# Kernel tuning notes

Hardware: AMD Instinct MI355X
Metric: run time of the kernel (lower is better)

## Reference

```python
import jax, jax.numpy as jnp
import numpy as np

NUM_HEAD_CHANNELS = 64
GROUPS = 32
EPS = 1e-5


def setup_inputs() -> dict:
    key = jax.random.key(0)
    ks = jax.random.split(key, 3)
    B, C, H, W = 16, 512, 64, 64
    x = jax.random.normal(ks[0], (B, C, H, W), jnp.float32)
    gn_gamma = jnp.ones((C,), jnp.float32)
    gn_beta = jnp.zeros((C,), jnp.float32)
    # 1x1 conv weights (out_ch, in_ch); fan-in scaling keeps softmax logits sane
    w_qkv = jax.random.normal(ks[1], (3 * C, C), jnp.float32) / np.float32(np.sqrt(C))
    b_qkv = jnp.zeros((3 * C,), jnp.float32)
    w_proj = jax.random.normal(ks[2], (C, C), jnp.float32) / np.float32(np.sqrt(C))
    b_proj = jnp.zeros((C,), jnp.float32)
    return dict(x=x, gn_gamma=gn_gamma, gn_beta=gn_beta, w_qkv=w_qkv,
                b_qkv=b_qkv, w_proj=w_proj, b_proj=b_proj)


def _group_norm(x, gamma, beta):
    B, C, H, W = x.shape
    xg = x.reshape(B, GROUPS, C // GROUPS, H, W)
    mu = xg.mean(axis=(2, 3, 4), keepdims=True)
    var = xg.var(axis=(2, 3, 4), keepdims=True)
    xn = ((xg - mu) * jax.lax.rsqrt(var + EPS)).reshape(B, C, H, W)
    return xn * gamma[None, :, None, None] + beta[None, :, None, None]


def reference(x, gn_gamma, gn_beta, w_qkv, b_qkv, w_proj, b_proj):
    B, C, H, W = x.shape
    L = H * W
    heads = C // NUM_HEAD_CHANNELS
    Lh = L // heads  # module splits spatial length across heads

    xn = _group_norm(x, gn_gamma, gn_beta).reshape(B, C, L)
    # 1x1 conv QKV: (3C, C) x (B, C, L) -> (B, 3C, L)
    qkv = jnp.einsum('oc,bcl->bol', w_qkv, xn) + b_qkv[None, :, None]
    qkv = qkv.reshape(B, 3 * C, heads, Lh)
    q, k, v = jnp.split(qkv, 3, axis=1)  # each (B, C, heads, Lh)

    scale = np.float32(1.0 / np.sqrt(C // heads))
    w_att = jnp.einsum('bchq,bchk->bhqk', q * scale, k)  # (B, heads, Lh, Lh)
    w_att = jax.nn.softmax(w_att.astype(jnp.float32), axis=-1).astype(q.dtype)
    a = jnp.einsum('bhqk,bchk->bchq', w_att, v)  # (B, C, heads, Lh)
    a = a.reshape(B, C, L)  # contiguous reinterpretation, as torch .view

    out = jnp.einsum('oc,bcl->bol', w_proj, a) + b_proj[None, :, None]
    return x + out.reshape(B, C, H, W)
```

## Files before the change

kernel.cpp:

```cpp
#include <hip/hip_runtime.h>

typedef unsigned short u16;
typedef __attribute__((ext_vector_type(8))) short bf16x8;
typedef __attribute__((ext_vector_type(4))) short bf16x4;
typedef __attribute__((ext_vector_type(4))) float f32x4;

__device__ __forceinline__ float bf2f(u16 u){ union { unsigned int i; float f; } v; v.i = ((unsigned int)u) << 16; return v.f; }
__device__ __forceinline__ u16 f2bf(float f){ union { float f; unsigned int i; } v; v.f = f; unsigned int r = v.i + 0x7fffu + ((v.i >> 16) & 1u); return (u16)(r >> 16); }

#define MFMA(a,b,c) __builtin_amdgcn_mfma_f32_16x16x32_bf16((a),(b),(c),0,0,0)

__device__ __forceinline__ void gl_lds16(const u16* g, u16* l){
  __builtin_amdgcn_global_load_lds((const __attribute__((address_space(1))) unsigned int*)g,
                                   (__attribute__((address_space(3))) unsigned int*)l, 16, 0, 0);
}

__global__ __launch_bounds__(256) void k_gn_stats(const float* __restrict__ x, float* __restrict__ stats){
  const int bg = blockIdx.x;
  const float4* p = (const float4*)(x + (size_t)bg * 65536);
  const int tid = threadIdx.x;
  float s = 0.f, sq = 0.f;
  for (int i = 0; i < 64; ++i){
    float4 v = p[tid + i*256];
    s += v.x + v.y + v.z + v.w;
    sq += v.x*v.x + v.y*v.y + v.z*v.z + v.w*v.w;
  }
#pragma unroll
  for (int d = 32; d > 0; d >>= 1){ s += __shfl_down(s, d, 64); sq += __shfl_down(sq, d, 64); }
  __shared__ float ls[4], lq[4];
  if ((tid & 63) == 0){ ls[tid>>6] = s; lq[tid>>6] = sq; }
  __syncthreads();
  if (tid == 0){
    float S = ls[0]+ls[1]+ls[2]+ls[3];
    float Q = lq[0]+lq[1]+lq[2]+lq[3];
    float mean = S * (1.f/65536.f);
    float var  = Q * (1.f/65536.f) - mean*mean;
    stats[bg*2]   = mean;
    stats[bg*2+1] = rsqrtf(var + 1e-5f);
  }
}

__global__ __launch_bounds__(256) void k_conv_w(const float* __restrict__ wq, const float* __restrict__ wp,
                                                u16* __restrict__ wout){
  const int base = (blockIdx.x*256 + threadIdx.x) * 4;
  float4 v;
  if (base < 786432) v = *(const float4*)(wq + base);
  else               v = *(const float4*)(wp + (base - 786432));
  bf16x4 o;
  o[0] = (short)f2bf(v.x); o[1] = (short)f2bf(v.y); o[2] = (short)f2bf(v.z); o[3] = (short)f2bf(v.w);
  *(bf16x4*)(wout + base) = o;
}

__global__ __launch_bounds__(256) void k_gn_t(const float* __restrict__ x, const float* __restrict__ stats,
                                              const float* __restrict__ gamma, const float* __restrict__ beta,
                                              u16* __restrict__ xnt){
  __shared__ u16 tile[64*72];
  const int l0 = blockIdx.x*64, c0 = blockIdx.y*64, b = blockIdx.z;
  const int tid = threadIdx.x;
#pragma unroll
  for (int i = 0; i < 2; ++i){
    int v = tid + i*256; int cc = v >> 3, seg = v & 7;
    int c = c0 + cc;
    float mu = stats[(b*32 + (c>>4))*2], rs = stats[(b*32 + (c>>4))*2 + 1];
    float ga = gamma[c] * rs;
    float be = beta[c] - mu * ga;
    const float* px = x + ((size_t)(b*512 + c))*4096 + l0 + seg*8;
    float4 a0 = *(const float4*)px;
    float4 a1 = *(const float4*)(px + 4);
    bf16x8 ov;
    ov[0]=(short)f2bf(a0.x*ga+be); ov[1]=(short)f2bf(a0.y*ga+be);
    ov[2]=(short)f2bf(a0.z*ga+be); ov[3]=(short)f2bf(a0.w*ga+be);
    ov[4]=(short)f2bf(a1.x*ga+be); ov[5]=(short)f2bf(a1.y*ga+be);
    ov[6]=(short)f2bf(a1.z*ga+be); ov[7]=(short)f2bf(a1.w*ga+be);
    *(bf16x8*)&tile[cc*72 + seg*8] = ov;
  }
  __syncthreads();
#pragma unroll
  for (int i = 0; i < 2; ++i){
    int v = tid + i*256; int ll = v >> 3, seg = v & 7;
    bf16x8 ov;
#pragma unroll
    for (int j = 0; j < 8; ++j) ov[j] = (short)tile[(seg*8 + j)*72 + ll];
    *(bf16x8*)(xnt + ((size_t)(b*4096 + l0 + ll))*512 + c0 + seg*8) = ov;
  }
}

__global__ __launch_bounds__(256,2) void k_qkv(const u16* __restrict__ xnt, const u16* __restrict__ wq,
                                               const float* __restrict__ bq,
                                               u16* __restrict__ Qt, u16* __restrict__ Kt, u16* __restrict__ Vh){
  __shared__ u16 smem[17408];
  u16* sA = smem;
  u16* sW = smem + 8192;
  const int l0 = blockIdx.x*128, o0 = blockIdx.y*128, b = blockIdx.z;
  const int tid = threadIdx.x, wv = tid>>6, lane = tid&63, g = lane>>4, r = lane&15;
  const int wm = wv>>1, wn = wv&1;
  const u16* Ab = xnt + ((size_t)(b*4096 + l0))*512;
  const u16* Wb = wq  + (size_t)o0*512;
  int srow[4], scol[4];
#pragma unroll
  for (int j = 0; j < 4; ++j){
    int s = wv*256 + j*64 + lane;
    srow[j] = s >> 3;
    scol[j] = ((s & 7) ^ (srow[j] & 7)) * 8;
  }
  f32x4 acc[4][4];
#pragma unroll
  for (int mt = 0; mt < 4; ++mt)
#pragma unroll
    for (int nt = 0; nt < 4; ++nt) acc[mt][nt] = (f32x4){0.f,0.f,0.f,0.f};

  const int key = r & 7;
  for (int c0 = 0; c0 < 512; c0 += 64){
    __syncthreads();
#pragma unroll
    for (int j = 0; j < 4; ++j){
      u16* ldst = &smem[(wv*256 + j*64)*8];
      gl_lds16(Ab + (size_t)srow[j]*512 + c0 + scol[j], ldst);
      gl_lds16(Wb + (size_t)srow[j]*512 + c0 + scol[j], ldst + 8192);
    }
    __syncthreads();
#pragma unroll
    for (int half = 0; half < 2; ++half){
      bf16x8 a[4], w[4];
#pragma unroll
      for (int mt = 0; mt < 4; ++mt){ int R = wm*64 + mt*16 + r; a[mt] = *(const bf16x8*)&sA[(R*8 + ((half*4+g) ^ key))*8]; }
#pragma unroll
      for (int nt = 0; nt < 4; ++nt){ int R = wn*64 + nt*16 + r; w[nt] = *(const bf16x8*)&sW[(R*8 + ((half*4+g) ^ key))*8]; }
#pragma unroll
      for (int mt = 0; mt < 4; ++mt)
#pragma unroll
        for (int nt = 0; nt < 4; ++nt) acc[mt][nt] = MFMA(a[mt], w[nt], acc[mt][nt]);
    }
  }
  __syncthreads();
  const int t   = blockIdx.y >> 2;
  const int cp0 = (blockIdx.y & 3)*128;
  const int h   = blockIdx.x >> 2;
  const int lh0 = (blockIdx.x & 3)*128;
#pragma unroll
  for (int nt = 0; nt < 4; ++nt){
    const int ol = wn*64 + nt*16 + r;
    const float bi = bq[o0 + ol];
#pragma unroll
    for (int mt = 0; mt < 4; ++mt){
      const int ll = wm*64 + mt*16 + g*4;
      if (t == 2){
        bf16x4 pk;
#pragma unroll
        for (int rr = 0; rr < 4; ++rr) pk[rr] = (short)f2bf(acc[mt][nt][rr] + bi);
        *(bf16x4*)&smem[ol*136 + ll] = pk;
      } else {
#pragma unroll
        for (int rr = 0; rr < 4; ++rr) smem[(ll + rr)*136 + ol] = f2bf(acc[mt][nt][rr] + bi);
      }
    }
  }
  __syncthreads();
  const size_t bh = (size_t)(b*8 + h);
  u16* dst = (t == 0) ? Qt : Kt;
#pragma unroll
  for (int i = 0; i < 8; ++i){
    int v = tid + i*256; int row = v >> 4, seg = v & 15;
    bf16x8 d = *(const bf16x8*)&smem[row*136 + seg*8];
    if (t == 2){
      *(bf16x8*)(Vh + (bh*512 + cp0 + row)*512 + lh0 + seg*8) = d;
    } else {
      *(bf16x8*)(dst + (bh*512 + lh0 + row)*512 + cp0 + seg*8) = d;
    }
  }
}

__global__ __launch_bounds__(512,2) void k_attn(const u16* __restrict__ Qt, const u16* __restrict__ Kt,
                                                const u16* __restrict__ Vh, u16* __restrict__ At){
  extern __shared__ __align__(16) u16 smem[];
  float* sMax = (float*)(smem + 65536);
  float* sSum = sMax + 512;
  const int q0 = blockIdx.x * 128;
  const int h = blockIdx.y, b = blockIdx.z;
  const int bh = b*8 + h;
  const int tid = threadIdx.x, wv = tid>>6, lane = tid&63, g = lane>>4, r = lane&15;
  const int wq = wv>>2, wk = wv&3;
  const size_t base = (size_t)bh * 262144;
  const u16* Qb = Qt + base + (size_t)q0*512;
  const u16* Kb = Kt + base;
  const u16* Vb = Vh + base;

  const u16* gsrc[5];
  int ldoff[5];
  {
    const int l4 = lane >> 2, pc = lane & 3;
#pragma unroll
    for (int j = 0; j < 5; ++j){
      const int i = wv*5 + j;
      const int row = ((i < 8) ? (i*16) : ((i-8)*16)) + l4;
      const u16* bp = (i < 8) ? (Qb + (size_t)row*512) : (Kb + (size_t)row*512);
      gsrc[j] = bp + ((pc ^ (row & 3)) * 8);
      ldoff[j] = i * 512;
    }
  }

  f32x4 s[4][8];
#pragma unroll
  for (int mt = 0; mt < 4; ++mt)
#pragma unroll
    for (int nt = 0; nt < 8; ++nt) s[mt][nt] = (f32x4){0.f,0.f,0.f,0.f};

  const int qswz = (g ^ (r & 3)) * 8;

#pragma unroll
  for (int j = 0; j < 5; ++j) gl_lds16(gsrc[j], smem + ldoff[j]);
  __syncthreads();
  for (int cs = 0; cs < 16; ++cs){
    u16* bb = smem + (cs & 1) * 20480;
    if (cs < 15){
      u16* bn = smem + ((cs + 1) & 1) * 20480;
      const int c0 = (cs + 1) * 32;
#pragma unroll
      for (int j = 0; j < 5; ++j) gl_lds16(gsrc[j] + c0, bn + ldoff[j]);
    }
    bf16x8 a[4], kb[8];
#pragma unroll
    for (int mt = 0; mt < 4; ++mt) a[mt] = *(const bf16x8*)&bb[(wq*64 + mt*16 + r)*32 + qswz];
#pragma unroll
    for (int nt = 0; nt < 8; ++nt) kb[nt] = *(const bf16x8*)&bb[4096 + (wk*128 + nt*16 + r)*32 + qswz];
#pragma unroll
    for (int mt = 0; mt < 4; ++mt)
#pragma unroll
      for (int nt = 0; nt < 8; ++nt) s[mt][nt] = MFMA(a[mt], kb[nt], s[mt][nt]);
    __syncthreads();
  }

#pragma unroll
  for (int mt = 0; mt < 4; ++mt)
#pragma unroll
    for (int nt = 0; nt < 8; ++nt)
#pragma unroll
      for (int rr = 0; rr < 4; ++rr) s[mt][nt][rr] *= 0.125f;

  float mx[4][4];
#pragma unroll
  for (int mt = 0; mt < 4; ++mt)
#pragma unroll
    for (int rr = 0; rr < 4; ++rr){
      float m = s[mt][0][rr];
#pragma unroll
      for (int nt = 1; nt < 8; ++nt) m = fmaxf(m, s[mt][nt][rr]);
      m = fmaxf(m, __shfl_xor(m, 1, 64)); m = fmaxf(m, __shfl_xor(m, 2, 64));
      m = fmaxf(m, __shfl_xor(m, 4, 64)); m = fmaxf(m, __shfl_xor(m, 8, 64));
      mx[mt][rr] = m;
    }
  if (r == 0){
#pragma unroll
    for (int mt = 0; mt < 4; ++mt)
#pragma unroll
      for (int rr = 0; rr < 4; ++rr) sMax[(wq*64 + mt*16 + g*4 + rr)*4 + wk] = mx[mt][rr];
  }
  __syncthreads();
#pragma unroll
  for (int mt = 0; mt < 4; ++mt)
#pragma unroll
    for (int rr = 0; rr < 4; ++rr){
      float4 v = *(const float4*)&sMax[(wq*64 + mt*16 + g*4 + rr)*4];
      mx[mt][rr] = fmaxf(fmaxf(v.x, v.y), fmaxf(v.z, v.w));
    }
  float inv[4][4];
#pragma unroll
  for (int mt = 0; mt < 4; ++mt)
#pragma unroll
    for (int rr = 0; rr < 4; ++rr){
      float t = 0.f;
#pragma unroll
      for (int nt = 0; nt < 8; ++nt){
        float e = __expf(s[mt][nt][rr] - mx[mt][rr]);
        s[mt][nt][rr] = e; t += e;
      }
      t += __shfl_xor(t, 1, 64); t += __shfl_xor(t, 2, 64);
      t += __shfl_xor(t, 4, 64); t += __shfl_xor(t, 8, 64);
      inv[mt][rr] = t;
    }
  if (r == 0){
#pragma unroll
    for (int mt = 0; mt < 4; ++mt)
#pragma unroll
      for (int rr = 0; rr < 4; ++rr) sSum[(wq*64 + mt*16 + g*4 + rr)*4 + wk] = inv[mt][rr];
  }
  __syncthreads();
#pragma unroll
  for (int mt = 0; mt < 4; ++mt)
#pragma unroll
    for (int rr = 0; rr < 4; ++rr){
      float4 v = *(const float4*)&sSum[(wq*64 + mt*16 + g*4 + rr)*4];
      inv[mt][rr] = 1.f / (v.x + v.y + v.z + v.w);
    }
  {
    const int kx7 = r & 7, kbase = wk*16 + (r>>3);
#pragma unroll
    for (int mt = 0; mt < 4; ++mt)
#pragma unroll
      for (int rr = 0; rr < 4; ++rr){
        const int q = wq*64 + mt*16 + g*4 + rr;
        const int ro = q*512, qx = q & 7;
        const float iv = inv[mt][rr];
#pragma unroll
        for (int nt = 0; nt < 8; ++nt){
          const int ch = kbase + nt*2;
          smem[ro + ((ch ^ qx) * 8) + kx7] = f2bf(s[mt][nt][rr] * iv);
        }
      }
  }
  __syncthreads();

  f32x4 o[4][8];
#pragma unroll
  for (int mt = 0; mt < 4; ++mt)
#pragma unroll
    for (int nt = 0; nt < 8; ++nt) o[mt][nt] = (f32x4){0.f,0.f,0.f,0.f};
  const u16* Vw = Vb + (size_t)(wv*64 + r)*512 + g*8;
  bf16x8 vf[2][4];
#pragma unroll
  for (int mt = 0; mt < 4; ++mt) vf[0][mt] = *(const bf16x8*)(Vw + mt*8192);
#pragma unroll
  for (int kk = 0; kk < 16; ++kk){
    if (kk < 15){
#pragma unroll
      for (int mt = 0; mt < 4; ++mt) vf[(kk+1)&1][mt] = *(const bf16x8*)(Vw + mt*8192 + (kk+1)*32);
    }
    bf16x8 pp[8];
#pragma unroll
    for (int nt = 0; nt < 8; ++nt){
      const int q = nt*16 + r;
      pp[nt] = *(const bf16x8*)&smem[q*512 + (((kk*4 + g) ^ (r & 7)) * 8)];
    }
#pragma unroll
    for (int mt = 0; mt < 4; ++mt)
#pragma unroll
      for (int nt = 0; nt < 8; ++nt) o[mt][nt] = MFMA(vf[kk&1][mt], pp[nt], o[mt][nt]);
  }
  __syncthreads();

#pragma unroll
  for (int mt = 0; mt < 4; ++mt){
    const int c = wv*64 + mt*16 + g*4;
    const int ch = c >> 3, cl = c & 7;
#pragma unroll
    for (int nt = 0; nt < 8; ++nt){
      const int q = nt*16 + r;
      bf16x4 pk;
#pragma unroll
      for (int rr = 0; rr < 4; ++rr) pk[rr] = (short)f2bf(o[mt][nt][rr]);
      *(bf16x4*)&smem[q*512 + ((ch ^ (r & 7)) * 8) + cl] = pk;
    }
  }
  __syncthreads();
  u16* Ad = At + ((size_t)(bh*512 + q0))*512;
#pragma unroll
  for (int i = 0; i < 16; ++i){
    const int idx = tid + i*512, q = idx >> 6, ch = idx & 63;
    bf16x8 d = *(const bf16x8*)&smem[q*512 + ((ch ^ (q & 7)) * 8)];
    *(bf16x8*)(Ad + (size_t)q*512 + ch*8) = d;
  }
}

__global__ __launch_bounds__(256,2) void k_proj(const u16* __restrict__ At, const u16* __restrict__ wp,
                                                const float* __restrict__ bpr, const float* __restrict__ x,
                                                float* __restrict__ out){
  __shared__ u16 smem[17408];
  u16* sA = smem;
  u16* sW = smem + 8192;
  const int l0 = blockIdx.x*128, o0 = blockIdx.y*128, b = blockIdx.z;
  const int tid = threadIdx.x, wv = tid>>6, lane = tid&63, g = lane>>4, r = lane&15;
  const int wm = wv>>1, wn = wv&1;
  const u16* Ab = At + ((size_t)(b*4096 + l0))*512;
  const u16* Wb = wp + (size_t)o0*512;
  int srow[4], scol[4];
#pragma unroll
  for (int j = 0; j < 4; ++j){
    int s = wv*256 + j*64 + lane;
    srow[j] = s >> 3;
    scol[j] = ((s & 7) ^ (srow[j] & 7)) * 8;
  }
  f32x4 acc[4][4];
#pragma unroll
  for (int mt = 0; mt < 4; ++mt)
#pragma unroll
    for (int nt = 0; nt < 4; ++nt) acc[mt][nt] = (f32x4){0.f,0.f,0.f,0.f};
  const int key = r & 7;
  for (int c0 = 0; c0 < 512; c0 += 64){
    __syncthreads();
#pragma unroll
    for (int j = 0; j < 4; ++j){
      u16* ldst = &smem[(wv*256 + j*64)*8];
      gl_lds16(Ab + (size_t)srow[j]*512 + c0 + scol[j], ldst);
      gl_lds16(Wb + (size_t)srow[j]*512 + c0 + scol[j], ldst + 8192);
    }
    __syncthreads();
#pragma unroll
    for (int half = 0; half < 2; ++half){
      bf16x8 a[4], w[4];
#pragma unroll
      for (int mt = 0; mt < 4; ++mt){ int R = wm*64 + mt*16 + r; a[mt] = *(const bf16x8*)&sA[(R*8 + ((half*4+g) ^ key))*8]; }
#pragma unroll
      for (int nt = 0; nt < 4; ++nt){ int R = wn*64 + nt*16 + r; w[nt] = *(const bf16x8*)&sW[(R*8 + ((half*4+g) ^ key))*8]; }
#pragma unroll
      for (int mt = 0; mt < 4; ++mt)
#pragma unroll
        for (int nt = 0; nt < 4; ++nt) acc[mt][nt] = MFMA(a[mt], w[nt], acc[mt][nt]);
    }
  }
  __syncthreads();
#pragma unroll
  for (int nt = 0; nt < 4; ++nt){
    const int ol = wn*64 + nt*16 + r;
    const float bi = bpr[o0 + ol];
#pragma unroll
    for (int mt = 0; mt < 4; ++mt){
      const int ll = wm*64 + mt*16 + g*4;
      bf16x4 pk;
#pragma unroll
      for (int rr = 0; rr < 4; ++rr) pk[rr] = (short)f2bf(acc[mt][nt][rr] + bi);
      *(bf16x4*)&smem[ol*136 + ll] = pk;
    }
  }
  __syncthreads();
#pragma unroll
  for (int i = 0; i < 16; ++i){
    int v = tid + i*256; int row = v >> 5, seg = v & 31;
    bf16x4 d = *(const bf16x4*)&smem[row*136 + seg*4];
    const size_t gi = ((size_t)(b*512 + o0 + row))*4096 + l0 + seg*4;
    float4 xv = *(const float4*)(x + gi);
    float4 ov;
    ov.x = bf2f((u16)d[0]) + xv.x;
    ov.y = bf2f((u16)d[1]) + xv.y;
    ov.z = bf2f((u16)d[2]) + xv.z;
    ov.w = bf2f((u16)d[3]) + xv.w;
    *(float4*)(out + gi) = ov;
  }
}

extern "C" void kernel_launch(void* const* d_in, const int* in_sizes, int n_in,
                              void* d_out, int out_size, void* d_ws, size_t ws_size,
                              hipStream_t stream) {
  (void)in_sizes; (void)n_in; (void)out_size; (void)ws_size;
  const float* x     = (const float*)d_in[0];
  const float* gamma = (const float*)d_in[1];
  const float* beta  = (const float*)d_in[2];
  const float* wqkv  = (const float*)d_in[3];
  const float* bqkv  = (const float*)d_in[4];
  const float* wproj = (const float*)d_in[5];
  const float* bproj = (const float*)d_in[6];
  float* out = (float*)d_out;
  char* ws = (char*)d_ws;

  float* stats = (float*)ws;
  u16* W16  = (u16*)(ws + 8192);
  u16* Wq16 = W16;
  u16* Wp16 = W16 + 786432;
  u16* Qt = (u16*)(ws + 8192 + 2097152);
  u16* Kt = Qt + (size_t)33554432;
  u16* Vh = Kt + (size_t)33554432;
  u16* At = Qt;
  u16* Xnt = (u16*)d_out;

  static bool attn_attr = false;
  if (!attn_attr){
    hipFuncSetAttribute((const void*)k_attn, hipFuncAttributeMaxDynamicSharedMemorySize, 135168);
    attn_attr = true;
  }

  k_gn_stats<<<512, 256, 0, stream>>>(x, stats);
  k_conv_w<<<1024, 256, 0, stream>>>(wqkv, wproj, W16);
  k_gn_t<<<dim3(64,8,16), 256, 0, stream>>>(x, stats, gamma, beta, Xnt);
  k_qkv<<<dim3(32,12,16), 256, 0, stream>>>(Xnt, Wq16, bqkv, Qt, Kt, Vh);
  k_attn<<<dim3(4,8,16), 512, 135168, stream>>>(Qt, Kt, Vh, At);
  k_proj<<<dim3(32,4,16), 256, 0, stream>>>(At, Wp16, bproj, x, out);
}
```

Before: 567.9 us.

## Triple-buffer QK staging, remap attention blocks across XCDs, raise MFMA priority

The QK^T loop moves from double to triple buffering. Async global-to-LDS loads are issued two stages ahead, and the code waits on an explicit vmcnt with a raw barrier instead of a full __syncthreads each step. The attention grid is flattened to 1D with a workgroup-id swizzle so blocks of the same batch/head land on the same XCD for L2 reuse of K/V. MFMA sections get s_setprio(1), and the first V fragment load is hoisted above the barrier before the PV loop. The intent is to hide load latency and sync overhead; the hand-set vmcnt depends on the exact count of outstanding loads being correct.

```diff
diff --git a/kernel.cpp b/kernel.cpp
--- a/kernel.cpp
+++ b/kernel.cpp
@@ -175,8 +175,9 @@
   extern __shared__ __align__(16) u16 smem[];
   float* sMax = (float*)(smem + 65536);
   float* sSum = sMax + 512;
-  const int q0 = blockIdx.x * 128;
-  const int h = blockIdx.y, b = blockIdx.z;
+  const int wgid = blockIdx.x;
+  const int orig = (wgid & 7)*64 + (wgid >> 3);
+  const int b = orig >> 5, h = (orig >> 2) & 7, q0 = (orig & 3) * 128;
   const int bh = b*8 + h;
   const int tid = threadIdx.x, wv = tid>>6, lane = tid&63, g = lane>>4, r = lane&15;
   const int wq = wv>>2, wk = wv&3;
@@ -207,28 +208,45 @@
 
   const int qswz = (g ^ (r & 3)) * 8;
 
-#pragma unroll
-  for (int j = 0; j < 5; ++j) gl_lds16(gsrc[j], smem + ldoff[j]);
-  __syncthreads();
-  for (int cs = 0; cs < 16; ++cs){
-    u16* bb = smem + (cs & 1) * 20480;
-    if (cs < 15){
-      u16* bn = smem + ((cs + 1) & 1) * 20480;
-      const int c0 = (cs + 1) * 32;
-#pragma unroll
-      for (int j = 0; j < 5; ++j) gl_lds16(gsrc[j] + c0, bn + ldoff[j]);
-    }
-    bf16x8 a[4], kb[8];
-#pragma unroll
-    for (int mt = 0; mt < 4; ++mt) a[mt] = *(const bf16x8*)&bb[(wq*64 + mt*16 + r)*32 + qswz];
-#pragma unroll
-    for (int nt = 0; nt < 8; ++nt) kb[nt] = *(const bf16x8*)&bb[4096 + (wk*128 + nt*16 + r)*32 + qswz];
-#pragma unroll
-    for (int mt = 0; mt < 4; ++mt)
-#pragma unroll
-      for (int nt = 0; nt < 8; ++nt) s[mt][nt] = MFMA(a[mt], kb[nt], s[mt][nt]);
-    __syncthreads();
-  }
+#define STAGE_QK(bufbase, c0) do { \
+    u16* _bb = (bufbase); \
+    _Pragma("unroll") \
+    for (int _j = 0; _j < 5; ++_j) gl_lds16(gsrc[_j] + (c0), _bb + ldoff[_j]); \
+  } while(0)
+
+#define QK_COMPUTE(bbp) do { \
+    const u16* _cb = (bbp); \
+    bf16x8 a_[4], kb_[8]; \
+    _Pragma("unroll") \
+    for (int _mt = 0; _mt < 4; ++_mt) a_[_mt] = *(const bf16x8*)&_cb[(wq*64 + _mt*16 + r)*32 + qswz]; \
+    _Pragma("unroll") \
+    for (int _nt = 0; _nt < 8; ++_nt) kb_[_nt] = *(const bf16x8*)&_cb[4096 + (wk*128 + _nt*16 + r)*32 + qswz]; \
+    __builtin_amdgcn_s_setprio(1); \
+    _Pragma("unroll") \
+    for (int _mt = 0; _mt < 4; ++_mt) \
+      _Pragma("unroll") \
+      for (int _nt = 0; _nt < 8; ++_nt) s[_mt][_nt] = MFMA(a_[_mt], kb_[_nt], s[_mt][_nt]); \
+    __builtin_amdgcn_s_setprio(0); \
+  } while(0)
+
+  STAGE_QK(smem,         0);
+  STAGE_QK(smem + 20480, 32);
+  int bcur = 0;
+  for (int cs = 0; cs < 15; ++cs){
+    asm volatile("s_waitcnt vmcnt(5)" ::: "memory");
+    __builtin_amdgcn_s_barrier();
+    __builtin_amdgcn_sched_barrier(0);
+    if (cs < 14){
+      int bn = bcur + 2; if (bn >= 3) bn -= 3;
+      STAGE_QK(smem + bn*20480, (cs+2)*32);
+    }
+    QK_COMPUTE(smem + bcur*20480);
+    if (++bcur == 3) bcur = 0;
+  }
+  asm volatile("s_waitcnt vmcnt(0)" ::: "memory");
+  __builtin_amdgcn_s_barrier();
+  __builtin_amdgcn_sched_barrier(0);
+  QK_COMPUTE(smem + bcur*20480);
 
 #pragma unroll
   for (int mt = 0; mt < 4; ++mt)
@@ -308,17 +326,17 @@
         }
       }
   }
-  __syncthreads();
-
-  f32x4 o[4][8];
-#pragma unroll
-  for (int mt = 0; mt < 4; ++mt)
-#pragma unroll
-    for (int nt = 0; nt < 8; ++nt) o[mt][nt] = (f32x4){0.f,0.f,0.f,0.f};
   const u16* Vw = Vb + (size_t)(wv*64 + r)*512 + g*8;
   bf16x8 vf[2][4];
 #pragma unroll
   for (int mt = 0; mt < 4; ++mt) vf[0][mt] = *(const bf16x8*)(Vw + mt*8192);
+  __syncthreads();
+
+  f32x4 o[4][8];
+#pragma unroll
+  for (int mt = 0; mt < 4; ++mt)
+#pragma unroll
+    for (int nt = 0; nt < 8; ++nt) o[mt][nt] = (f32x4){0.f,0.f,0.f,0.f};
 #pragma unroll
   for (int kk = 0; kk < 16; ++kk){
     if (kk < 15){
@@ -331,10 +349,12 @@
       const int q = nt*16 + r;
       pp[nt] = *(const bf16x8*)&smem[q*512 + (((kk*4 + g) ^ (r & 7)) * 8)];
     }
+    __builtin_amdgcn_s_setprio(1);
 #pragma unroll
     for (int mt = 0; mt < 4; ++mt)
 #pragma unroll
       for (int nt = 0; nt < 8; ++nt) o[mt][nt] = MFMA(vf[kk&1][mt], pp[nt], o[mt][nt]);
+    __builtin_amdgcn_s_setprio(0);
   }
   __syncthreads();
 
@@ -359,6 +379,8 @@
     bf16x8 d = *(const bf16x8*)&smem[q*512 + ((ch ^ (q & 7)) * 8)];
     *(bf16x8*)(Ad + (size_t)q*512 + ch*8) = d;
   }
+#undef STAGE_QK
+#undef QK_COMPUTE
 }
 
 __global__ __launch_bounds__(256,2) void k_proj(const u16* __restrict__ At, const u16* __restrict__ wp,
@@ -471,6 +493,6 @@
   k_conv_w<<<1024, 256, 0, stream>>>(wqkv, wproj, W16);
   k_gn_t<<<dim3(64,8,16), 256, 0, stream>>>(x, stats, gamma, beta, Xnt);
   k_qkv<<<dim3(32,12,16), 256, 0, stream>>>(Xnt, Wq16, bqkv, Qt, Kt, Vh);
-  k_attn<<<dim3(4,8,16), 512, 135168, stream>>>(Qt, Kt, Vh, At);
+  k_attn<<<512, 512, 135168, stream>>>(Qt, Kt, Vh, At);
   k_proj<<<dim3(32,4,16), 256, 0, stream>>>(At, Wp16, bproj, x, out);
 }
```

New measurement: 545.7 us. 3.9% less time.

## Shrink attention tile to 64 queries, raise occupancy, fuse prep kernels

Applied to the files above, without the earlier changes.

The attention kernel now processes 64 queries per workgroup instead of 128. Each wave owns 64 keys and reads K directly from global memory, while only Q is staged through LDS. Dynamic shared memory drops from 135168 to 77824 bytes and the launch bound rises to 4 workgroups per CU, aiming for higher occupancy and more grid parallelism. A remapped 1D grid with an XCD-style workgroup swizzle and s_setprio around the MFMA blocks are added. The GN-stats and weight-conversion kernels are also merged into one launch. The risks are more global K/V traffic, since each workgroup rereads full K and V for fewer queries, and extra barriers per Q chunk.

```diff
diff --git a/kernel.cpp b/kernel.cpp
--- a/kernel.cpp
+++ b/kernel.cpp
@@ -15,40 +15,41 @@
                                    (__attribute__((address_space(3))) unsigned int*)l, 16, 0, 0);
 }
 
-__global__ __launch_bounds__(256) void k_gn_stats(const float* __restrict__ x, float* __restrict__ stats){
-  const int bg = blockIdx.x;
-  const float4* p = (const float4*)(x + (size_t)bg * 65536);
+__global__ __launch_bounds__(256) void k_prep(const float* __restrict__ x, float* __restrict__ stats,
+                                              const float* __restrict__ wq, const float* __restrict__ wp,
+                                              u16* __restrict__ wout){
+  __shared__ float ls[4], lq[4];
   const int tid = threadIdx.x;
-  float s = 0.f, sq = 0.f;
-  for (int i = 0; i < 64; ++i){
-    float4 v = p[tid + i*256];
-    s += v.x + v.y + v.z + v.w;
-    sq += v.x*v.x + v.y*v.y + v.z*v.z + v.w*v.w;
-  }
-#pragma unroll
-  for (int d = 32; d > 0; d >>= 1){ s += __shfl_down(s, d, 64); sq += __shfl_down(sq, d, 64); }
-  __shared__ float ls[4], lq[4];
-  if ((tid & 63) == 0){ ls[tid>>6] = s; lq[tid>>6] = sq; }
-  __syncthreads();
-  if (tid == 0){
-    float S = ls[0]+ls[1]+ls[2]+ls[3];
-    float Q = lq[0]+lq[1]+lq[2]+lq[3];
-    float mean = S * (1.f/65536.f);
-    float var  = Q * (1.f/65536.f) - mean*mean;
-    stats[bg*2]   = mean;
-    stats[bg*2+1] = rsqrtf(var + 1e-5f);
-  }
-}
-
-__global__ __launch_bounds__(256) void k_conv_w(const float* __restrict__ wq, const float* __restrict__ wp,
-                                                u16* __restrict__ wout){
-  const int base = (blockIdx.x*256 + threadIdx.x) * 4;
-  float4 v;
-  if (base < 786432) v = *(const float4*)(wq + base);
-  else               v = *(const float4*)(wp + (base - 786432));
-  bf16x4 o;
-  o[0] = (short)f2bf(v.x); o[1] = (short)f2bf(v.y); o[2] = (short)f2bf(v.z); o[3] = (short)f2bf(v.w);
-  *(bf16x4*)(wout + base) = o;
+  if (blockIdx.x < 512){
+    const int bg = blockIdx.x;
+    const float4* p = (const float4*)(x + (size_t)bg * 65536);
+    float s = 0.f, sq = 0.f;
+    for (int i = 0; i < 64; ++i){
+      float4 v = p[tid + i*256];
+      s += v.x + v.y + v.z + v.w;
+      sq += v.x*v.x + v.y*v.y + v.z*v.z + v.w*v.w;
+    }
+#pragma unroll
+    for (int d = 32; d > 0; d >>= 1){ s += __shfl_down(s, d, 64); sq += __shfl_down(sq, d, 64); }
+    if ((tid & 63) == 0){ ls[tid>>6] = s; lq[tid>>6] = sq; }
+    __syncthreads();
+    if (tid == 0){
+      float S = ls[0]+ls[1]+ls[2]+ls[3];
+      float Q = lq[0]+lq[1]+lq[2]+lq[3];
+      float mean = S * (1.f/65536.f);
+      float var  = Q * (1.f/65536.f) - mean*mean;
+      stats[bg*2]   = mean;
+      stats[bg*2+1] = rsqrtf(var + 1e-5f);
+    }
+  } else {
+    const int base = ((blockIdx.x - 512)*256 + tid) * 4;
+    float4 v;
+    if (base < 786432) v = *(const float4*)(wq + base);
+    else               v = *(const float4*)(wp + (base - 786432));
+    bf16x4 o;
+    o[0] = (short)f2bf(v.x); o[1] = (short)f2bf(v.y); o[2] = (short)f2bf(v.z); o[3] = (short)f2bf(v.w);
+    *(bf16x4*)(wout + base) = o;
+  }
 }
 
 __global__ __launch_bounds__(256) void k_gn_t(const float* __restrict__ x, const float* __restrict__ stats,
@@ -170,70 +171,59 @@
   }
 }
 
-__global__ __launch_bounds__(512,2) void k_attn(const u16* __restrict__ Qt, const u16* __restrict__ Kt,
+__global__ __launch_bounds__(512,4) void k_attn(const u16* __restrict__ Qt, const u16* __restrict__ Kt,
                                                 const u16* __restrict__ Vh, u16* __restrict__ At){
   extern __shared__ __align__(16) u16 smem[];
-  float* sMax = (float*)(smem + 65536);
+  u16*  sQ   = smem + 32768;
+  float* sMax = (float*)(smem + 36864);
   float* sSum = sMax + 512;
-  const int q0 = blockIdx.x * 128;
-  const int h = blockIdx.y, b = blockIdx.z;
+  const int wgid = blockIdx.x;
+  const int orig = (wgid & 7)*128 + (wgid >> 3);
+  const int b = orig >> 6, h = (orig >> 3) & 7, q0 = (orig & 7) * 64;
   const int bh = b*8 + h;
   const int tid = threadIdx.x, wv = tid>>6, lane = tid&63, g = lane>>4, r = lane&15;
-  const int wq = wv>>2, wk = wv&3;
   const size_t base = (size_t)bh * 262144;
   const u16* Qb = Qt + base + (size_t)q0*512;
   const u16* Kb = Kt + base;
   const u16* Vb = Vh + base;
 
-  const u16* gsrc[5];
-  int ldoff[5];
-  {
-    const int l4 = lane >> 2, pc = lane & 3;
-#pragma unroll
-    for (int j = 0; j < 5; ++j){
-      const int i = wv*5 + j;
-      const int row = ((i < 8) ? (i*16) : ((i-8)*16)) + l4;
-      const u16* bp = (i < 8) ? (Qb + (size_t)row*512) : (Kb + (size_t)row*512);
-      gsrc[j] = bp + ((pc ^ (row & 3)) * 8);
-      ldoff[j] = i * 512;
-    }
-  }
-
-  f32x4 s[4][8];
-#pragma unroll
-  for (int mt = 0; mt < 4; ++mt)
-#pragma unroll
-    for (int nt = 0; nt < 8; ++nt) s[mt][nt] = (f32x4){0.f,0.f,0.f,0.f};
-
-  const int qswz = (g ^ (r & 3)) * 8;
-
-#pragma unroll
-  for (int j = 0; j < 5; ++j) gl_lds16(gsrc[j], smem + ldoff[j]);
-  __syncthreads();
-  for (int cs = 0; cs < 16; ++cs){
-    u16* bb = smem + (cs & 1) * 20480;
-    if (cs < 15){
-      u16* bn = smem + ((cs + 1) & 1) * 20480;
-      const int c0 = (cs + 1) * 32;
-#pragma unroll
-      for (int j = 0; j < 5; ++j) gl_lds16(gsrc[j] + c0, bn + ldoff[j]);
-    }
-    bf16x8 a[4], kb[8];
-#pragma unroll
-    for (int mt = 0; mt < 4; ++mt) a[mt] = *(const bf16x8*)&bb[(wq*64 + mt*16 + r)*32 + qswz];
-#pragma unroll
-    for (int nt = 0; nt < 8; ++nt) kb[nt] = *(const bf16x8*)&bb[4096 + (wk*128 + nt*16 + r)*32 + qswz];
-#pragma unroll
-    for (int mt = 0; mt < 4; ++mt)
-#pragma unroll
-      for (int nt = 0; nt < 8; ++nt) s[mt][nt] = MFMA(a[mt], kb[nt], s[mt][nt]);
-    __syncthreads();
-  }
-
-#pragma unroll
-  for (int mt = 0; mt < 4; ++mt)
-#pragma unroll
-    for (int nt = 0; nt < 8; ++nt)
+  const int qrow = tid >> 3;
+  const u16* qsrc = Qb + (size_t)qrow*512 + (((tid & 7) ^ (qrow & 7)) * 8);
+  u16* qdst = sQ + wv*512;
+
+  f32x4 s[4][4];
+#pragma unroll
+  for (int mt = 0; mt < 4; ++mt)
+#pragma unroll
+    for (int nt = 0; nt < 4; ++nt) s[mt][nt] = (f32x4){0.f,0.f,0.f,0.f};
+
+  const int key = r & 7;
+  for (int cs = 0; cs < 8; ++cs){
+    const int c0 = cs * 64;
+    __syncthreads();
+    gl_lds16(qsrc + c0, qdst);
+    __syncthreads();
+#pragma unroll
+    for (int half = 0; half < 2; ++half){
+      bf16x8 a[4], kb[4];
+#pragma unroll
+      for (int nt = 0; nt < 4; ++nt)
+        kb[nt] = *(const bf16x8*)(Kb + (size_t)(wv*64 + nt*16 + r)*512 + c0 + half*32 + g*8);
+#pragma unroll
+      for (int mt = 0; mt < 4; ++mt){ int R = mt*16 + r; a[mt] = *(const bf16x8*)&sQ[(R*8 + ((half*4+g) ^ key))*8]; }
+      __builtin_amdgcn_s_setprio(1);
+#pragma unroll
+      for (int mt = 0; mt < 4; ++mt)
+#pragma unroll
+        for (int nt = 0; nt < 4; ++nt) s[mt][nt] = MFMA(a[mt], kb[nt], s[mt][nt]);
+      __builtin_amdgcn_s_setprio(0);
+    }
+  }
+
+#pragma unroll
+  for (int mt = 0; mt < 4; ++mt)
+#pragma unroll
+    for (int nt = 0; nt < 4; ++nt)
 #pragma unroll
       for (int rr = 0; rr < 4; ++rr) s[mt][nt][rr] *= 0.125f;
 
@@ -244,7 +234,7 @@
     for (int rr = 0; rr < 4; ++rr){
       float m = s[mt][0][rr];
 #pragma unroll
-      for (int nt = 1; nt < 8; ++nt) m = fmaxf(m, s[mt][nt][rr]);
+      for (int nt = 1; nt < 4; ++nt) m = fmaxf(m, s[mt][nt][rr]);
       m = fmaxf(m, __shfl_xor(m, 1, 64)); m = fmaxf(m, __shfl_xor(m, 2, 64));
       m = fmaxf(m, __shfl_xor(m, 4, 64)); m = fmaxf(m, __shfl_xor(m, 8, 64));
       mx[mt][rr] = m;
@@ -253,15 +243,18 @@
 #pragma unroll
     for (int mt = 0; mt < 4; ++mt)
 #pragma unroll
-      for (int rr = 0; rr < 4; ++rr) sMax[(wq*64 + mt*16 + g*4 + rr)*4 + wk] = mx[mt][rr];
+      for (int rr = 0; rr < 4; ++rr) sMax[(mt*16 + g*4 + rr)*8 + wv] = mx[mt][rr];
   }
   __syncthreads();
 #pragma unroll
   for (int mt = 0; mt < 4; ++mt)
 #pragma unroll
     for (int rr = 0; rr < 4; ++rr){
-      float4 v = *(const float4*)&sMax[(wq*64 + mt*16 + g*4 + rr)*4];
-      mx[mt][rr] = fmaxf(fmaxf(v.x, v.y), fmaxf(v.z, v.w));
+      const int q = mt*16 + g*4 + rr;
+      float4 v0 = *(const float4*)&sMax[q*8];
+      float4 v1 = *(const float4*)&sMax[q*8 + 4];
+      mx[mt][rr] = fmaxf(fmaxf(fmaxf(v0.x, v0.y), fmaxf(v0.z, v0.w)),
+                         fmaxf(fmaxf(v1.x, v1.y), fmaxf(v1.z, v1.w)));
     }
   float inv[4][4];
 #pragma unroll
@@ -270,7 +263,7 @@
     for (int rr = 0; rr < 4; ++rr){
       float t = 0.f;
 #pragma unroll
-      for (int nt = 0; nt < 8; ++nt){
+      for (int nt = 0; nt < 4; ++nt){
         float e = __expf(s[mt][nt][rr] - mx[mt][rr]);
         s[mt][nt][rr] = e; t += e;
       }
@@ -282,59 +275,63 @@
 #pragma unroll
     for (int mt = 0; mt < 4; ++mt)
 #pragma unroll
-      for (int rr = 0; rr < 4; ++rr) sSum[(wq*64 + mt*16 + g*4 + rr)*4 + wk] = inv[mt][rr];
+      for (int rr = 0; rr < 4; ++rr) sSum[(mt*16 + g*4 + rr)*8 + wv] = inv[mt][rr];
   }
   __syncthreads();
 #pragma unroll
   for (int mt = 0; mt < 4; ++mt)
 #pragma unroll
     for (int rr = 0; rr < 4; ++rr){
-      float4 v = *(const float4*)&sSum[(wq*64 + mt*16 + g*4 + rr)*4];
-      inv[mt][rr] = 1.f / (v.x + v.y + v.z + v.w);
+      const int q = mt*16 + g*4 + rr;
+      float4 v0 = *(const float4*)&sSum[q*8];
+      float4 v1 = *(const float4*)&sSum[q*8 + 4];
+      inv[mt][rr] = 1.f / (v0.x + v0.y + v0.z + v0.w + v1.x + v1.y + v1.z + v1.w);
     }
   {
-    const int kx7 = r & 7, kbase = wk*16 + (r>>3);
+    const int kx7 = r & 7, chb = wv*8 + (r >> 3);
 #pragma unroll
     for (int mt = 0; mt < 4; ++mt)
 #pragma unroll
       for (int rr = 0; rr < 4; ++rr){
-        const int q = wq*64 + mt*16 + g*4 + rr;
+        const int q = mt*16 + g*4 + rr;
         const int ro = q*512, qx = q & 7;
         const float iv = inv[mt][rr];
 #pragma unroll
-        for (int nt = 0; nt < 8; ++nt){
-          const int ch = kbase + nt*2;
+        for (int nt = 0; nt < 4; ++nt){
+          const int ch = chb + nt*2;
           smem[ro + ((ch ^ qx) * 8) + kx7] = f2bf(s[mt][nt][rr] * iv);
         }
       }
   }
-  __syncthreads();
-
-  f32x4 o[4][8];
-#pragma unroll
-  for (int mt = 0; mt < 4; ++mt)
-#pragma unroll
-    for (int nt = 0; nt < 8; ++nt) o[mt][nt] = (f32x4){0.f,0.f,0.f,0.f};
   const u16* Vw = Vb + (size_t)(wv*64 + r)*512 + g*8;
   bf16x8 vf[2][4];
 #pragma unroll
   for (int mt = 0; mt < 4; ++mt) vf[0][mt] = *(const bf16x8*)(Vw + mt*8192);
+  __syncthreads();
+
+  f32x4 o[4][4];
+#pragma unroll
+  for (int mt = 0; mt < 4; ++mt)
+#pragma unroll
+    for (int nt = 0; nt < 4; ++nt) o[mt][nt] = (f32x4){0.f,0.f,0.f,0.f};
 #pragma unroll
   for (int kk = 0; kk < 16; ++kk){
     if (kk < 15){
 #pragma unroll
       for (int mt = 0; mt < 4; ++mt) vf[(kk+1)&1][mt] = *(const bf16x8*)(Vw + mt*8192 + (kk+1)*32);
     }
-    bf16x8 pp[8];
-#pragma unroll
-    for (int nt = 0; nt < 8; ++nt){
+    bf16x8 pp[4];
+#pragma unroll
+    for (int nt = 0; nt < 4; ++nt){
       const int q = nt*16 + r;
       pp[nt] = *(const bf16x8*)&smem[q*512 + (((kk*4 + g) ^ (r & 7)) * 8)];
     }
+    __builtin_amdgcn_s_setprio(1);
 #pragma unroll
     for (int mt = 0; mt < 4; ++mt)
 #pragma unroll
-      for (int nt = 0; nt < 8; ++nt) o[mt][nt] = MFMA(vf[kk&1][mt], pp[nt], o[mt][nt]);
+      for (int nt = 0; nt < 4; ++nt) o[mt][nt] = MFMA(vf[kk&1][mt], pp[nt], o[mt][nt]);
+    __builtin_amdgcn_s_setprio(0);
   }
   __syncthreads();
 
@@ -343,7 +340,7 @@
     const int c = wv*64 + mt*16 + g*4;
     const int ch = c >> 3, cl = c & 7;
 #pragma unroll
-    for (int nt = 0; nt < 8; ++nt){
+    for (int nt = 0; nt < 4; ++nt){
       const int q = nt*16 + r;
       bf16x4 pk;
 #pragma unroll
@@ -354,7 +351,7 @@
   __syncthreads();
   u16* Ad = At + ((size_t)(bh*512 + q0))*512;
 #pragma unroll
-  for (int i = 0; i < 16; ++i){
+  for (int i = 0; i < 8; ++i){
     const int idx = tid + i*512, q = idx >> 6, ch = idx & 63;
     bf16x8 d = *(const bf16x8*)&smem[q*512 + ((ch ^ (q & 7)) * 8)];
     *(bf16x8*)(Ad + (size_t)q*512 + ch*8) = d;
@@ -463,14 +460,13 @@
 
   static bool attn_attr = false;
   if (!attn_attr){
-    hipFuncSetAttribute((const void*)k_attn, hipFuncAttributeMaxDynamicSharedMemorySize, 135168);
+    hipFuncSetAttribute((const void*)k_attn, hipFuncAttributeMaxDynamicSharedMemorySize, 77824);
     attn_attr = true;
   }
 
-  k_gn_stats<<<512, 256, 0, stream>>>(x, stats);
-  k_conv_w<<<1024, 256, 0, stream>>>(wqkv, wproj, W16);
+  k_prep<<<1536, 256, 0, stream>>>(x, stats, wqkv, wproj, W16);
   k_gn_t<<<dim3(64,8,16), 256, 0, stream>>>(x, stats, gamma, beta, Xnt);
   k_qkv<<<dim3(32,12,16), 256, 0, stream>>>(Xnt, Wq16, bqkv, Qt, Kt, Vh);
-  k_attn<<<dim3(4,8,16), 512, 135168, stream>>>(Qt, Kt, Vh, At);
+  k_attn<<<1024, 512, 77824, stream>>>(Qt, Kt, Vh, At);
   k_proj<<<dim3(32,4,16), 256, 0, stream>>>(At, Wp16, bproj, x, out);
 }
```

Result: slower. 627.7 us (+10.5%).
